# Kernel tuning notes

Measured on AMD Instinct MI355X. Metric: run time of the kernel, lower is better.

The kernel has to match this reference:

```python
import jax, jax.numpy as jnp
import numpy as np

B, T, E, H = 8, 2048, 1024, 64

def setup_inputs() -> dict:
    key = jax.random.key(0)
    ks = jax.random.split(key, 7)
    s = 1.0 / np.sqrt(E)
    return {
        "x": jax.random.normal(ks[0], (B, T, E), dtype=jnp.float32),
        "Wk": jax.random.normal(ks[1], (E, H), dtype=jnp.float32) * s,
        "bk": jax.random.normal(ks[2], (H,), dtype=jnp.float32) * 0.01,
        "Wq": jax.random.normal(ks[3], (E, H), dtype=jnp.float32) * s,
        "bq": jax.random.normal(ks[4], (H,), dtype=jnp.float32) * 0.01,
        "Wv": jax.random.normal(ks[5], (E, H), dtype=jnp.float32) * s,
        "bv": jax.random.normal(ks[6], (H,), dtype=jnp.float32) * 0.01,
    }

def reference(x, Wk, bk, Wq, bq, Wv, bv):
    # q,k,v: [B, T, H]
    k = x @ Wk + bk
    q = x @ Wq + bq
    v = x @ Wv + bv
    scale = jnp.asarray(H, x.dtype) ** -0.5
    scores = jnp.einsum('bth,bsh->bts', q, k) * scale  # [B, T, T]
    T_ = x.shape[1]
    causal = jnp.tril(jnp.ones((T_, T_), dtype=bool))
    scores = jnp.where(causal, scores, jnp.asarray(-jnp.inf, x.dtype))
    attn = jax.nn.softmax(scores, axis=-1)  # dropout p=0.0 -> identity
    return jnp.einsum('bts,bsh->bth', attn, v)
```

## Files before the change

### kernel.cpp

```cpp
#include <hip/hip_runtime.h>
#include <hip/hip_bf16.h>
#include <math.h>

#define BB 8
#define TT 2048
#define EE 1024
#define HH 64
#define QSCALE 0.18033688011112042f

typedef __attribute__((ext_vector_type(8))) short short8;
typedef __attribute__((ext_vector_type(4))) float f32x4;
typedef __attribute__((ext_vector_type(16))) float f32x16;
typedef __attribute__((ext_vector_type(4))) unsigned short us4;

__device__ inline unsigned short f2bf(float f) {
  union { __hip_bfloat16 h; unsigned short u; } cv;
  cv.h = __float2bfloat16(f);
  return cv.u;
}

__global__ __launch_bounds__(256) void prep_w(
    const float* __restrict__ Wk, const float* __restrict__ Wq,
    const float* __restrict__ Wv, unsigned short* __restrict__ Wf) {
  const int idx = blockIdx.x * 256 + threadIdx.x;
  const int lane = idx & 63, ks = (idx >> 6) & 31, t = idx >> 11;
  const int q = lane & 15, g = lane >> 4;
  const int m = t >> 2, h = (t & 3) * 16 + q;
  const float* W = (m == 0) ? Wk : (m == 1) ? Wq : Wv;
  const float sc = (m == 1) ? QSCALE : 1.f;
  const int e0 = ks * 32 + g * 8;
  unsigned short v[8];
  #pragma unroll
  for (int j = 0; j < 8; ++j) v[j] = f2bf(W[(e0 + j) * 64 + h] * sc);
  *(short8*)&Wf[(size_t)idx * 8] = *(short8*)v;
}

__global__ __launch_bounds__(256) void qkv_proj(
    const float* __restrict__ x,
    const float* __restrict__ bk, const float* __restrict__ bq,
    const float* __restrict__ bv, const unsigned short* __restrict__ Wf,
    unsigned short* __restrict__ kf, unsigned short* __restrict__ qf,
    unsigned short* __restrict__ vf) {
  __shared__ alignas(16) unsigned short xs[2][32][264];

  const int tid = threadIdx.x;
  const long row0 = (long)blockIdx.x * 32;
  const int w = tid >> 6, lane = tid & 63;
  const int q = lane & 15, g = lane >> 4;

  const float4* xg = (const float4*)&x[row0 * EE];

  #pragma unroll
  for (int i = 0; i < 8; ++i) {
    const int flat = i * 256 + tid;
    const int rr = flat >> 6, c4 = flat & 63;
    const float4 xv = xg[rr * 256 + c4];
    us4 pk = {f2bf(xv.x), f2bf(xv.y), f2bf(xv.z), f2bf(xv.w)};
    *(us4*)&xs[0][rr][c4 * 4] = pk;
  }
  __syncthreads();

  const f32x4 z = {0.f, 0.f, 0.f, 0.f};
  f32x4 acc00 = z, acc01 = z, acc02 = z;
  f32x4 acc10 = z, acc11 = z, acc12 = z;
  const unsigned short* wf0 = &Wf[(size_t)(3 * w) * 16384 + (size_t)lane * 8];

  float4 st[8];
  #pragma unroll
  for (int cc = 0; cc < 4; ++cc) {
    if (cc < 3) {
      #pragma unroll
      for (int i = 0; i < 8; ++i) {
        const int flat = i * 256 + tid;
        const int rr = flat >> 6, c4 = flat & 63;
        st[i] = xg[rr * 256 + (cc + 1) * 64 + c4];
      }
    }
    #pragma unroll
    for (int ksl = 0; ksl < 8; ++ksl) {
      const short8 a0 = *(const short8*)&xs[cc & 1][q][ksl * 32 + g * 8];
      const short8 a1 = *(const short8*)&xs[cc & 1][16 + q][ksl * 32 + g * 8];
      const int ks = cc * 8 + ksl;
      const short8 b0 = *(const short8*)&wf0[ks * 512];
      const short8 b1 = *(const short8*)&wf0[16384 + ks * 512];
      const short8 b2 = *(const short8*)&wf0[32768 + ks * 512];
      acc00 = __builtin_amdgcn_mfma_f32_16x16x32_bf16(a0, b0, acc00, 0, 0, 0);
      acc10 = __builtin_amdgcn_mfma_f32_16x16x32_bf16(a1, b0, acc10, 0, 0, 0);
      acc01 = __builtin_amdgcn_mfma_f32_16x16x32_bf16(a0, b1, acc01, 0, 0, 0);
      acc11 = __builtin_amdgcn_mfma_f32_16x16x32_bf16(a1, b1, acc11, 0, 0, 0);
      acc02 = __builtin_amdgcn_mfma_f32_16x16x32_bf16(a0, b2, acc02, 0, 0, 0);
      acc12 = __builtin_amdgcn_mfma_f32_16x16x32_bf16(a1, b2, acc12, 0, 0, 0);
    }
    if (cc < 3) {
      #pragma unroll
      for (int i = 0; i < 8; ++i) {
        const int flat = i * 256 + tid;
        const int rr = flat >> 6, c4 = flat & 63;
        us4 pk = {f2bf(st[i].x), f2bf(st[i].y), f2bf(st[i].z), f2bf(st[i].w)};
        *(us4*)&xs[(cc + 1) & 1][rr][c4 * 4] = pk;
      }
    }
    __syncthreads();
  }

  unsigned short* img = (unsigned short*)xs;
  #pragma unroll
  for (int i = 0; i < 3; ++i) {
    const int tgl = 3 * w + i;
    const int mm = tgl >> 2, hb = tgl & 3;
    const int h = hb * 16 + q;
    const float bias = (mm == 0) ? bk[h] : (mm == 1) ? bq[h] * QSCALE : bv[h];
    #pragma unroll
    for (int stp = 0; stp < 2; ++stp) {
      const f32x4 a = (stp == 0) ? ((i == 0) ? acc00 : (i == 1) ? acc01 : acc02)
                                 : ((i == 0) ? acc10 : (i == 1) ? acc11 : acc12);
      #pragma unroll
      for (int r = 0; r < 4; ++r) {
        const int tl5 = stp * 16 + 4 * g + r;
        const unsigned short ov = f2bf(a[r] + bias);
        if (mm == 2) {
          const int lane32v = ((hb & 1) * 16 + q) + 32 * ((tl5 >> 3) & 1);
          img[4096 + (hb >> 1) * 1024 + ((tl5 >> 4) & 1) * 512 +
              lane32v * 8 + (tl5 & 7)] = ov;
        } else {
          const int lane32 = tl5 + 32 * ((q >> 3) & 1);
          img[mm * 2048 + hb * 512 + lane32 * 8 + (q & 7)] = ov;
        }
      }
    }
  }
  __syncthreads();
  const size_t obase = (size_t)(row0 >> 11) * 131072 +
                       (size_t)((row0 & 2047) >> 5) * 2048;
  const int o = tid * 8;
  *(short8*)&kf[obase + o] = *(const short8*)&img[o];
  *(short8*)&qf[obase + o] = *(const short8*)&img[2048 + o];
  *(short8*)&vf[obase + o] = *(const short8*)&img[4096 + o];
}

#define BODY(KC, KN, tt, PREF) do {                                          \
    const unsigned short* vp_ = vfb + (size_t)(tt) * 2048;                   \
    const short8 V00 = *(const short8*)&vp_[0];                              \
    const short8 V10 = *(const short8*)&vp_[1024];                           \
    if (PREF) {                                                              \
      const unsigned short* kp_ = kfb + (size_t)((tt) + stride) * 2048;      \
      KN[0] = *(const short8*)&kp_[0];                                       \
      KN[1] = *(const short8*)&kp_[512];                                     \
      KN[2] = *(const short8*)&kp_[1024];                                    \
      KN[3] = *(const short8*)&kp_[1536];                                    \
    }                                                                        \
    f32x16 S;                                                                \
    _Pragma("unroll")                                                        \
    for (int r = 0; r < 16; ++r) S[r] = 0.f;                                 \
    __builtin_amdgcn_s_setprio(1);                                           \
    S = __builtin_amdgcn_mfma_f32_32x32x16_bf16(KC[0], Qf0, S, 0, 0, 0);     \
    S = __builtin_amdgcn_mfma_f32_32x32x16_bf16(KC[1], Qf1, S, 0, 0, 0);     \
    S = __builtin_amdgcn_mfma_f32_32x32x16_bf16(KC[2], Qf2, S, 0, 0, 0);     \
    S = __builtin_amdgcn_mfma_f32_32x32x16_bf16(KC[3], Qf3, S, 0, 0, 0);     \
    __builtin_amdgcn_s_setprio(0);                                           \
    const int k0_ = (tt) * 32;                                               \
    if (k0_ + 31 > q0) {                                                     \
      _Pragma("unroll")                                                      \
      for (int r = 0; r < 16; ++r) {                                         \
        const int key = (r & 3) + 8 * (r >> 2) + 4 * hf;                     \
        if (k0_ + key > qg) S[r] = -INFINITY;                                \
      }                                                                      \
    }                                                                        \
    float pmax = S[0];                                                       \
    _Pragma("unroll")                                                        \
    for (int r = 1; r < 16; ++r) pmax = fmaxf(pmax, S[r]);                   \
    if (!__all(pmax <= m + 8.0f)) {                                          \
      const float pm2 = fmaxf(pmax, __shfl_xor(pmax, 32));                   \
      const float nm = fmaxf(m, pm2);                                        \
      const float rs = __builtin_amdgcn_exp2f(m - nm);                       \
      l *= rs;                                                               \
      _Pragma("unroll")                                                      \
      for (int r = 0; r < 16; ++r) { O0[r] *= rs; O1[r] *= rs; }             \
      m = nm;                                                                \
    }                                                                        \
    float ps = 0.f;                                                          \
    _Pragma("unroll")                                                        \
    for (int r = 0; r < 16; ++r) {                                           \
      S[r] = __builtin_amdgcn_exp2f(S[r] - m); ps += S[r];                   \
    }                                                                        \
    l += ps;                                                                 \
    unsigned wa0, wa1, wa2, wa3, wb0, wb1, wb2, wb3;                         \
    asm("v_cvt_pk_bf16_f32 %0, %1, %2" : "=v"(wa0) : "v"(S[0]), "v"(S[1])); \
    asm("v_cvt_pk_bf16_f32 %0, %1, %2" : "=v"(wb0) : "v"(S[2]), "v"(S[3])); \
    asm("v_cvt_pk_bf16_f32 %0, %1, %2" : "=v"(wa1) : "v"(S[4]), "v"(S[5])); \
    asm("v_cvt_pk_bf16_f32 %0, %1, %2" : "=v"(wb1) : "v"(S[6]), "v"(S[7])); \
    asm("v_cvt_pk_bf16_f32 %0, %1, %2" : "=v"(wa2) : "v"(S[8]), "v"(S[9])); \
    asm("v_cvt_pk_bf16_f32 %0, %1, %2" : "=v"(wb2) : "v"(S[10]), "v"(S[11]));\
    asm("v_cvt_pk_bf16_f32 %0, %1, %2" : "=v"(wa3) : "v"(S[12]), "v"(S[13]));\
    asm("v_cvt_pk_bf16_f32 %0, %1, %2" : "=v"(wb3) : "v"(S[14]), "v"(S[15]));\
    {                                  \
      const unsigned sA = hf ? wa1 : wa0, sB = hf ? wb1 : wb0;               \
      const unsigned tA = hf ? wa0 : wa1, tB = hf ? wb0 : wb1;               \
      const unsigned xA = __shfl_xor((int)tA, 32);                           \
      const unsigned xB = __shfl_xor((int)tB, 32);                           \
      union { unsigned u[4]; short8 s; } pf_;                                \
      pf_.u[0] = hf ? xA : sA; pf_.u[1] = hf ? xB : sB;                      \
      pf_.u[2] = hf ? sA : xA; pf_.u[3] = hf ? sB : xB;                      \
      __builtin_amdgcn_s_setprio(1);                                         \
      O0 = __builtin_amdgcn_mfma_f32_32x32x16_bf16(V00, pf_.s, O0, 0, 0, 0); \
      O1 = __builtin_amdgcn_mfma_f32_32x32x16_bf16(V10, pf_.s, O1, 0, 0, 0); \
      __builtin_amdgcn_s_setprio(0);                                         \
    }                                                                        \
    {                                                  \
      const short8 V01 = *(const short8*)&vp_[512];                          \
      const short8 V11 = *(const short8*)&vp_[1536];                         \
      const unsigned sA = hf ? wa3 : wa2, sB = hf ? wb3 : wb2;               \
      const unsigned tA = hf ? wa2 : wa3, tB = hf ? wb2 : wb3;               \
      const unsigned xA = __shfl_xor((int)tA, 32);                           \
      const unsigned xB = __shfl_xor((int)tB, 32);                           \
      union { unsigned u[4]; short8 s; } pf_;                                \
      pf_.u[0] = hf ? xA : sA; pf_.u[1] = hf ? xB : sB;                      \
      pf_.u[2] = hf ? sA : xA; pf_.u[3] = hf ? sB : xB;                      \
      __builtin_amdgcn_s_setprio(1);                                         \
      O0 = __builtin_amdgcn_mfma_f32_32x32x16_bf16(V01, pf_.s, O0, 0, 0, 0); \
      O1 = __builtin_amdgcn_mfma_f32_32x32x16_bf16(V11, pf_.s, O1, 0, 0, 0); \
      __builtin_amdgcn_s_setprio(0);                                         \
    }                                                                        \
  } while (0)

__global__ __launch_bounds__(1024, 4) void attn_fwd(
    const unsigned short* __restrict__ qf, const unsigned short* __restrict__ kf,
    const unsigned short* __restrict__ vf, float* __restrict__ out) {
  __shared__ float accS[16][32][65];
  __shared__ float mlS[16][2][32];

  const int tid = threadIdx.x;
  const int w = tid >> 6, lane = tid & 63;
  const int q = lane & 31, hf = lane >> 5;

  const int b = blockIdx.x & 7;
  const int p = blockIdx.x >> 3;
  const int s1 = 63 - p;
  const int nt0 = p + 1, nt1 = 64 - p;
  int k = (16 * nt0 + 32) / 65;
  if (k < 1) k = 1;
  if (k > 15) k = 15;

  const bool onS0 = (w < k);
  const int s = onS0 ? p : s1;
  const int nt = onS0 ? nt0 : nt1;
  const int stride = onS0 ? k : (16 - k);
  int t = onS0 ? w : (w - k);

  const int q0 = s * 32;
  const int qg = q0 + q;

  const unsigned short* kfb = kf + (size_t)b * 131072 + (size_t)lane * 8;
  const unsigned short* vfb = vf + (size_t)b * 131072 + (size_t)lane * 8;
  const unsigned short* qfb = qf + (size_t)b * 131072 + (size_t)s * 2048 +
                              (size_t)lane * 8;
  const short8 Qf0 = *(const short8*)&qfb[0];
  const short8 Qf1 = *(const short8*)&qfb[512];
  const short8 Qf2 = *(const short8*)&qfb[1024];
  const short8 Qf3 = *(const short8*)&qfb[1536];

  float m = -3.0e38f, l = 0.f;
  f32x16 O0, O1;
  #pragma unroll
  for (int r = 0; r < 16; ++r) { O0[r] = 0.f; O1[r] = 0.f; }

  {
    short8 A[4], B[4];
    const unsigned short* kp0 = kfb + (size_t)t * 2048;
    A[0] = *(const short8*)&kp0[0];
    A[1] = *(const short8*)&kp0[512];
    A[2] = *(const short8*)&kp0[1024];
    A[3] = *(const short8*)&kp0[1536];
    for (;;) {
      bool pf = (t + stride) < nt;
      BODY(A, B, t, pf);
      if (!pf) break;
      t += stride;
      pf = (t + stride) < nt;
      BODY(B, A, t, pf);
      if (!pf) break;
      t += stride;
    }
  }

  const float lq = l + __shfl_xor(l, 32);
  #pragma unroll
  for (int r = 0; r < 16; ++r) {
    const int hh0 = (r & 3) + 8 * (r >> 2) + 4 * hf;
    accS[w][q][hh0] = O0[r];
    accS[w][q][hh0 + 32] = O1[r];
  }
  if (hf == 0) { mlS[w][0][q] = m; mlS[w][1][q] = lq; }
  __syncthreads();

  const int half_t = tid >> 9;
  const int sm = half_t ? s1 : p;
  const int lo = half_t ? k : 0, hi2 = half_t ? 16 : k;
  const int idx = tid & 511;
  const int hh = idx & 63;
  const int qb0 = idx >> 6;
  const long obase = ((long)b * TT + (long)sm * 32) * 64;
  #pragma unroll
  for (int kk = 0; kk < 4; ++kk) {
    const int qv = qb0 + 8 * kk;
    float M = -INFINITY;
    for (int i = lo; i < hi2; ++i) M = fmaxf(M, mlS[i][0][qv]);
    float L = 0.f, acc = 0.f;
    for (int i = lo; i < hi2; ++i) {
      const float fi = __builtin_amdgcn_exp2f(mlS[i][0][qv] - M);
      L += fi * mlS[i][1][qv];
      acc += fi * accS[i][qv][hh];
    }
    out[obase + (long)qv * 64 + hh] = acc / L;
  }
}

extern "C" void kernel_launch(void* const* d_in, const int* in_sizes, int n_in,
                              void* d_out, int out_size, void* d_ws, size_t ws_size,
                              hipStream_t stream) {
  const float* x  = (const float*)d_in[0];
  const float* Wk = (const float*)d_in[1];
  const float* bk = (const float*)d_in[2];
  const float* Wq = (const float*)d_in[3];
  const float* bq = (const float*)d_in[4];
  const float* Wv = (const float*)d_in[5];
  const float* bv = (const float*)d_in[6];
  float* out = (float*)d_out;

  unsigned short* qfb = (unsigned short*)d_ws;
  unsigned short* kfb = qfb + (size_t)1048576;
  unsigned short* vfb = kfb + (size_t)1048576;
  unsigned short* Wf  = vfb + (size_t)1048576;

  prep_w<<<dim3(96), 256, 0, stream>>>(Wk, Wq, Wv, Wf);
  qkv_proj<<<dim3(512), 256, 0, stream>>>(x, bk, bq, bv, Wf, kfb, qfb, vfb);
  attn_fwd<<<dim3(256), 1024, 0, stream>>>(qfb, kfb, vfb, out);
}
```

Before: 52.35 us.

## Shrink QKV projection tiles to 16 rows and load x directly into MFMA registers

The projection kernel now handles 16 rows per block instead of 32 and launches twice as many blocks. Each wave computes one 16-column head block for K, Q and V, and the LDS staging of x is removed. Lanes read x straight from global memory into MFMA A-fragments, converting with packed bf16 conversion instructions. This drops the LDS round trip and the per-chunk barriers and adds parallelism. In exchange, each block re-reads the weights for half as many rows, and the strided per-lane loads of x may coalesce less well.

```diff
diff --git a/kernel.cpp b/kernel.cpp
--- a/kernel.cpp
+++ b/kernel.cpp
@@ -41,101 +41,76 @@
     const float* __restrict__ bv, const unsigned short* __restrict__ Wf,
     unsigned short* __restrict__ kf, unsigned short* __restrict__ qf,
     unsigned short* __restrict__ vf) {
-  __shared__ alignas(16) unsigned short xs[2][32][264];
+  __shared__ alignas(16) unsigned short img[3072];
 
   const int tid = threadIdx.x;
-  const long row0 = (long)blockIdx.x * 32;
+  const long row0 = (long)blockIdx.x * 16;
   const int w = tid >> 6, lane = tid & 63;
   const int q = lane & 15, g = lane >> 4;
 
-  const float4* xg = (const float4*)&x[row0 * EE];
-
-  #pragma unroll
-  for (int i = 0; i < 8; ++i) {
-    const int flat = i * 256 + tid;
-    const int rr = flat >> 6, c4 = flat & 63;
-    const float4 xv = xg[rr * 256 + c4];
-    us4 pk = {f2bf(xv.x), f2bf(xv.y), f2bf(xv.z), f2bf(xv.w)};
-    *(us4*)&xs[0][rr][c4 * 4] = pk;
-  }
-  __syncthreads();
+  const float* xr = x + (row0 + q) * EE + g * 8;
+  const unsigned short* wf0 = &Wf[(size_t)w * 16384 + (size_t)lane * 8];
 
   const f32x4 z = {0.f, 0.f, 0.f, 0.f};
-  f32x4 acc00 = z, acc01 = z, acc02 = z;
-  f32x4 acc10 = z, acc11 = z, acc12 = z;
-  const unsigned short* wf0 = &Wf[(size_t)(3 * w) * 16384 + (size_t)lane * 8];
-
-  float4 st[8];
-  #pragma unroll
-  for (int cc = 0; cc < 4; ++cc) {
-    if (cc < 3) {
-      #pragma unroll
-      for (int i = 0; i < 8; ++i) {
-        const int flat = i * 256 + tid;
-        const int rr = flat >> 6, c4 = flat & 63;
-        st[i] = xg[rr * 256 + (cc + 1) * 64 + c4];
+  f32x4 acc0 = z, acc1 = z, acc2 = z;
+
+  #pragma unroll 4
+  for (int ks = 0; ks < 32; ++ks) {
+    const float4 fa = *(const float4*)&xr[ks * 32];
+    const float4 fb = *(const float4*)&xr[ks * 32 + 4];
+    unsigned p0, p1, p2, p3;
+    asm("v_cvt_pk_bf16_f32 %0, %1, %2" : "=v"(p0) : "v"(fa.x), "v"(fa.y));
+    asm("v_cvt_pk_bf16_f32 %0, %1, %2" : "=v"(p1) : "v"(fa.z), "v"(fa.w));
+    asm("v_cvt_pk_bf16_f32 %0, %1, %2" : "=v"(p2) : "v"(fb.x), "v"(fb.y));
+    asm("v_cvt_pk_bf16_f32 %0, %1, %2" : "=v"(p3) : "v"(fb.z), "v"(fb.w));
+    union { unsigned u[4]; short8 s; } af;
+    af.u[0] = p0; af.u[1] = p1; af.u[2] = p2; af.u[3] = p3;
+    const short8 b0 = *(const short8*)&wf0[ks * 512];
+    const short8 b1 = *(const short8*)&wf0[65536 + ks * 512];
+    const short8 b2 = *(const short8*)&wf0[131072 + ks * 512];
+    acc0 = __builtin_amdgcn_mfma_f32_16x16x32_bf16(af.s, b0, acc0, 0, 0, 0);
+    acc1 = __builtin_amdgcn_mfma_f32_16x16x32_bf16(af.s, b1, acc1, 0, 0, 0);
+    acc2 = __builtin_amdgcn_mfma_f32_16x16x32_bf16(af.s, b2, acc2, 0, 0, 0);
+  }
+
+  const int h = w * 16 + q;
+  const float biask = bk[h], biasq = bq[h] * QSCALE, biasv = bv[h];
+  const int tl0 = (int)(row0 & 31);
+  #pragma unroll
+  for (int i = 0; i < 3; ++i) {
+    const f32x4 a = (i == 0) ? acc0 : (i == 1) ? acc1 : acc2;
+    const float bias = (i == 0) ? biask : (i == 1) ? biasq : biasv;
+    #pragma unroll
+    for (int r = 0; r < 4; ++r) {
+      const int tlh = 4 * g + r;
+      const unsigned short ov = f2bf(a[r] + bias);
+      if (i == 2) {
+        const int lane32v = ((w & 1) * 16 + q) + 32 * ((tlh >> 3) & 1);
+        img[2048 + (w >> 1) * 512 + lane32v * 8 + (tlh & 7)] = ov;
+      } else {
+        const int u = (q >> 3) & 1;
+        img[i * 1024 + w * 256 + u * 128 + tlh * 8 + (q & 7)] = ov;
       }
     }
-    #pragma unroll
-    for (int ksl = 0; ksl < 8; ++ksl) {
-      const short8 a0 = *(const short8*)&xs[cc & 1][q][ksl * 32 + g * 8];
-      const short8 a1 = *(const short8*)&xs[cc & 1][16 + q][ksl * 32 + g * 8];
-      const int ks = cc * 8 + ksl;
-      const short8 b0 = *(const short8*)&wf0[ks * 512];
-      const short8 b1 = *(const short8*)&wf0[16384 + ks * 512];
-      const short8 b2 = *(const short8*)&wf0[32768 + ks * 512];
-      acc00 = __builtin_amdgcn_mfma_f32_16x16x32_bf16(a0, b0, acc00, 0, 0, 0);
-      acc10 = __builtin_amdgcn_mfma_f32_16x16x32_bf16(a1, b0, acc10, 0, 0, 0);
-      acc01 = __builtin_amdgcn_mfma_f32_16x16x32_bf16(a0, b1, acc01, 0, 0, 0);
-      acc11 = __builtin_amdgcn_mfma_f32_16x16x32_bf16(a1, b1, acc11, 0, 0, 0);
-      acc02 = __builtin_amdgcn_mfma_f32_16x16x32_bf16(a0, b2, acc02, 0, 0, 0);
-      acc12 = __builtin_amdgcn_mfma_f32_16x16x32_bf16(a1, b2, acc12, 0, 0, 0);
-    }
-    if (cc < 3) {
-      #pragma unroll
-      for (int i = 0; i < 8; ++i) {
-        const int flat = i * 256 + tid;
-        const int rr = flat >> 6, c4 = flat & 63;
-        us4 pk = {f2bf(st[i].x), f2bf(st[i].y), f2bf(st[i].z), f2bf(st[i].w)};
-        *(us4*)&xs[(cc + 1) & 1][rr][c4 * 4] = pk;
-      }
-    }
-    __syncthreads();
-  }
-
-  unsigned short* img = (unsigned short*)xs;
-  #pragma unroll
-  for (int i = 0; i < 3; ++i) {
-    const int tgl = 3 * w + i;
-    const int mm = tgl >> 2, hb = tgl & 3;
-    const int h = hb * 16 + q;
-    const float bias = (mm == 0) ? bk[h] : (mm == 1) ? bq[h] * QSCALE : bv[h];
-    #pragma unroll
-    for (int stp = 0; stp < 2; ++stp) {
-      const f32x4 a = (stp == 0) ? ((i == 0) ? acc00 : (i == 1) ? acc01 : acc02)
-                                 : ((i == 0) ? acc10 : (i == 1) ? acc11 : acc12);
-      #pragma unroll
-      for (int r = 0; r < 4; ++r) {
-        const int tl5 = stp * 16 + 4 * g + r;
-        const unsigned short ov = f2bf(a[r] + bias);
-        if (mm == 2) {
-          const int lane32v = ((hb & 1) * 16 + q) + 32 * ((tl5 >> 3) & 1);
-          img[4096 + (hb >> 1) * 1024 + ((tl5 >> 4) & 1) * 512 +
-              lane32v * 8 + (tl5 & 7)] = ov;
-        } else {
-          const int lane32 = tl5 + 32 * ((q >> 3) & 1);
-          img[mm * 2048 + hb * 512 + lane32 * 8 + (q & 7)] = ov;
-        }
-      }
-    }
   }
   __syncthreads();
-  const size_t obase = (size_t)(row0 >> 11) * 131072 +
-                       (size_t)((row0 & 2047) >> 5) * 2048;
-  const int o = tid * 8;
-  *(short8*)&kf[obase + o] = *(const short8*)&img[o];
-  *(short8*)&qf[obase + o] = *(const short8*)&img[2048 + o];
-  *(short8*)&vf[obase + o] = *(const short8*)&img[4096 + o];
+
+  const size_t tb = (size_t)(row0 >> 11) * 131072 +
+                    (size_t)((row0 & 2047) >> 5) * 2048;
+  const int ks0v = tl0 >> 4;
+  if (tid < 128) {
+    const int hb = tid >> 5, u = (tid >> 4) & 1, l16 = tid & 15;
+    *(short8*)&kf[tb + hb * 512 + (l16 + tl0 + 32 * u) * 8] =
+        *(const short8*)&img[tid * 8];
+    const int hv = tid >> 6, ll = tid & 63;
+    *(short8*)&vf[tb + hv * 1024 + ks0v * 512 + ll * 8] =
+        *(const short8*)&img[2048 + tid * 8];
+  } else if (tid < 256) {
+    const int t2 = tid - 128;
+    const int hb = t2 >> 5, u = (t2 >> 4) & 1, l16 = t2 & 15;
+    *(short8*)&qf[tb + hb * 512 + (l16 + tl0 + 32 * u) * 8] =
+        *(const short8*)&img[1024 + t2 * 8];
+  }
 }
 
 #define BODY(KC, KN, tt, PREF) do {                                          \
@@ -333,6 +308,6 @@
   unsigned short* Wf  = vfb + (size_t)1048576;
 
   prep_w<<<dim3(96), 256, 0, stream>>>(Wk, Wq, Wv, Wf);
-  qkv_proj<<<dim3(512), 256, 0, stream>>>(x, bk, bq, bv, Wf, kfb, qfb, vfb);
+  qkv_proj<<<dim3(1024), 256, 0, stream>>>(x, bk, bq, bv, Wf, kfb, qfb, vfb);
   attn_fwd<<<dim3(256), 1024, 0, stream>>>(qfb, kfb, vfb, out);
 }
```

Result: slower. 70.35 us (+34.4%).
